# Kernel optimization log

Measured on AMD Instinct MI355X. Metric: run time of the kernel, lower is better.

The kernel has to match this reference:

```python
import jax, jax.numpy as jnp
import numpy as np

N = 65536      # bs * n_graphs * 32 electrodes
E = 1048576    # edges (avg degree 16)
H = 128        # first_hc (out_channels of GatedGraphConv)
IN = 5         # input node features
G = 16         # n_graphs (conv1d in-channels)
ELEC = 32
BS = 128
NC = 3


def setup_inputs() -> dict:
    key = jax.random.key(0)
    ks = jax.random.split(key, 14)
    s = 1.0 / np.sqrt(H)
    x = jax.random.normal(ks[0], (N, IN), dtype=jnp.float32)
    edge_index = jax.random.randint(ks[1], (2, E), 0, N, dtype=jnp.int32)
    edge_attr = jax.random.uniform(ks[2], (E,), dtype=jnp.float32)
    gconv_w = jax.random.normal(ks[3], (2, H, H), dtype=jnp.float32) * s
    gru_w_ih = jax.random.normal(ks[4], (3 * H, H), dtype=jnp.float32) * s
    gru_w_hh = jax.random.normal(ks[5], (3 * H, H), dtype=jnp.float32) * s
    gru_b_ih = jax.random.normal(ks[6], (3 * H,), dtype=jnp.float32) * s
    gru_b_hh = jax.random.normal(ks[7], (3 * H,), dtype=jnp.float32) * s
    conv_w = jax.random.normal(ks[8], (1, G, 3), dtype=jnp.float32) * (1.0 / np.sqrt(G * 3))
    conv_b = jax.random.normal(ks[9], (1,), dtype=jnp.float32) * 0.1
    L = (H - 3) // 2 + 1  # 63
    lin1_w = jax.random.normal(ks[10], (H, ELEC * L), dtype=jnp.float32) * (1.0 / np.sqrt(ELEC * L))
    lin1_b = jnp.zeros((H,), dtype=jnp.float32)
    lin2_w = jax.random.normal(ks[11], (NC, H), dtype=jnp.float32) * s
    lin2_b = jnp.zeros((NC,), dtype=jnp.float32)
    return {"x": x, "edge_index": edge_index, "edge_attr": edge_attr, "bs": BS,
            "gconv_w": gconv_w, "gru_w_ih": gru_w_ih, "gru_w_hh": gru_w_hh,
            "gru_b_ih": gru_b_ih, "gru_b_hh": gru_b_hh,
            "conv_w": conv_w, "conv_b": conv_b,
            "lin1_w": lin1_w, "lin1_b": lin1_b, "lin2_w": lin2_w, "lin2_b": lin2_b}


def _gated_graph_conv(x, edge_index, edge_attr, gconv_w, w_ih, w_hh, b_ih, b_hh):
    n = x.shape[0]
    # pad input features up to H (PyG GatedGraphConv behavior when in < out)
    h = jnp.concatenate([x, jnp.zeros((n, H - x.shape[1]), dtype=x.dtype)], axis=1)
    src, dst = edge_index[0], edge_index[1]
    for i in range(2):  # num_layers = 2
        m = h @ gconv_w[i]                              # [N, H]
        msg = m[src] * edge_attr[:, None]               # gather + edge weight
        agg = jax.ops.segment_sum(msg, dst, num_segments=n)  # scatter-add
        # GRUCell(agg, h)
        gi = agg @ w_ih.T + b_ih
        gh = h @ w_hh.T + b_hh
        i_r, i_z, i_n = jnp.split(gi, 3, axis=1)
        h_r, h_z, h_n = jnp.split(gh, 3, axis=1)
        r = jax.nn.sigmoid(i_r + h_r)
        z = jax.nn.sigmoid(i_z + h_z)
        nn_ = jnp.tanh(i_n + r * h_n)
        h = (1.0 - z) * nn_ + z * h
    return h


def reference(x, edge_index, edge_attr, bs, gconv_w, gru_w_ih, gru_w_hh,
              gru_b_ih, gru_b_hh, conv_w, conv_b, lin1_w, lin1_b, lin2_w, lin2_b):
    h = _gated_graph_conv(x, edge_index, edge_attr, gconv_w,
                          gru_w_ih, gru_w_hh, gru_b_ih, gru_b_hh)
    h = jax.nn.relu(h)  # dropout is identity in eval mode
    g = h.shape[0] // (bs * ELEC)
    # (bs g e) f -> (bs e) g f
    h = h.reshape(bs, g, ELEC, H).transpose(0, 2, 1, 3).reshape(bs * ELEC, g, H)
    h = jax.lax.conv_general_dilated(h, conv_w, window_strides=(2,), padding='VALID',
                                     dimension_numbers=('NCH', 'OIH', 'NCH'))
    h = h + conv_b[None, :, None]
    h = jax.nn.relu(h[:, 0, :])                 # squeeze channel -> [bs*e, L]
    h = h.reshape(bs, -1)                       # (bs e) f -> bs (e f)
    h = jax.nn.relu(h @ lin1_w.T + lin1_b)
    h = h @ lin2_w.T + lin2_b
    return jax.nn.softmax(h, axis=-1)
```

## Files before the change

### kernel.cpp

```cpp
#include <hip/hip_runtime.h>
#include <math.h>

#define NN 65536
#define NE 1048576
#define HH 128
#define ELEC 32
#define BSZ 128
#define NB 512

typedef unsigned short ushort_t;
typedef __bf16 bf16x8 __attribute__((ext_vector_type(8)));
typedef float f32x16 __attribute__((ext_vector_type(16)));

#define MFMA(A, B, C) __builtin_amdgcn_mfma_f32_32x32x16_bf16(A, B, C, 0, 0, 0)

__device__ __forceinline__ float sigm(float x) { return 1.f / (1.f + __expf(-x)); }
__device__ __forceinline__ float tanh_fast(float x) { return 2.f / (1.f + __expf(-2.f * x)) - 1.f; }

__device__ __forceinline__ float bf2f(ushort_t u) {
    union { unsigned int i; float f; } v; v.i = ((unsigned int)u) << 16; return v.f;
}
__device__ __forceinline__ ushort_t f2bf(float f) {
    union { float f; unsigned int i; } v; v.f = f;
    unsigned int r = (v.i + 0x7fffu + ((v.i >> 16) & 1u)) >> 16;
    return (ushort_t)r;
}


__global__ void k_init(const float* __restrict__ x, ushort_t* __restrict__ h) {
    int i = blockIdx.x * 256 + threadIdx.x;
    int n = i >> 7, c = i & 127;
    float v = (c < 5) ? x[n * 5 + c] : 0.f;
    h[(size_t)n * 128 + c] = f2bf(v);
}

__global__ __launch_bounds__(256) void k_bhist(const int* __restrict__ dst,
                                               int* __restrict__ bcnt) {
    __shared__ int hh[NB];
    int t = threadIdx.x;
    hh[t] = 0; hh[t + 256] = 0;
    __syncthreads();
    int e0 = blockIdx.x * 4096;
    #pragma unroll
    for (int i = 0; i < 16; ++i)
        atomicAdd(&hh[dst[e0 + i * 256 + t] >> 7], 1);
    __syncthreads();
    int c0 = hh[t];       if (c0) atomicAdd(&bcnt[t], c0);
    int c1 = hh[t + 256]; if (c1) atomicAdd(&bcnt[t + 256], c1);
}

__global__ void k_bscan(const int* __restrict__ bcnt, int* __restrict__ boffs,
                        int* __restrict__ bcur) {
    __shared__ int s[NB];
    int t = threadIdx.x;
    int v = bcnt[t];
    s[t] = v;
    __syncthreads();
    for (int d = 1; d < NB; d <<= 1) {
        int u = (t >= d) ? s[t - d] : 0;
        __syncthreads();
        s[t] += u;
        __syncthreads();
    }
    int ex = s[t] - v;
    boffs[t] = ex;
    bcur[t] = ex;
    if (t == NB - 1) boffs[NB] = s[t];
}

__global__ __launch_bounds__(256) void k_bpart(const int* __restrict__ src,
        const int* __restrict__ dst, const float* __restrict__ ea,
        int* __restrict__ bcur, uint2* __restrict__ ebkt) {
    __shared__ int lcnt[NB];
    __shared__ int base[NB];
    __shared__ int lcur[NB];
    int t = threadIdx.x;
    lcnt[t] = 0; lcnt[t + 256] = 0;
    lcur[t] = 0; lcur[t + 256] = 0;
    __syncthreads();
    int e0 = blockIdx.x * 4096;
    #pragma unroll
    for (int i = 0; i < 16; ++i)
        atomicAdd(&lcnt[dst[e0 + i * 256 + t] >> 7], 1);
    __syncthreads();
    {
        int c = lcnt[t];
        base[t] = c ? atomicAdd(&bcur[t], c) : 0;
        c = lcnt[t + 256];
        base[t + 256] = c ? atomicAdd(&bcur[t + 256], c) : 0;
    }
    __syncthreads();
    #pragma unroll
    for (int i = 0; i < 16; ++i) {
        int e = e0 + i * 256 + t;
        int d = dst[e];
        int bk = d >> 7;
        int pos = base[bk] + atomicAdd(&lcur[bk], 1);
        uint2 pk;
        pk.x = (unsigned int)src[e] | ((unsigned int)(d & 127) << 16);
        pk.y = __float_as_uint(ea[e]);
        ebkt[pos] = pk;
    }
}

__global__ __launch_bounds__(256) void k_csc(const int* __restrict__ boffs,
        const uint2* __restrict__ ebkt, uint2* __restrict__ epack,
        int* __restrict__ offs) {
    __shared__ int cnt[128];
    __shared__ int s[128];
    __shared__ int base[128];
    int b = blockIdx.x, t = threadIdx.x;
    if (t < 128) cnt[t] = 0;
    __syncthreads();
    int e0 = boffs[b], e1 = boffs[b + 1];
    for (int i = e0 + t; i < e1; i += 256)
        atomicAdd(&cnt[(ebkt[i].x >> 16) & 127], 1);
    __syncthreads();
    if (t < 128) s[t] = cnt[t];
    __syncthreads();
    for (int d = 1; d < 128; d <<= 1) {
        int v = (t < 128 && t >= d) ? s[t - d] : 0;
        __syncthreads();
        if (t < 128) s[t] += v;
        __syncthreads();
    }
    if (t < 128) {
        int bs = e0 + s[t] - cnt[t];
        base[t] = bs;
        offs[b * 128 + t] = bs;
        cnt[t] = 0;
    }
    if (b == 0 && t == 255) offs[NN] = NE;
    __syncthreads();
    for (int i = e0 + t; i < e1; i += 256) {
        uint2 e = ebkt[i];
        int dl = (e.x >> 16) & 127;
        int pos = base[dl] + atomicAdd(&cnt[dl], 1);
        epack[pos] = e;
    }
}

__global__ void k_prep(const float* __restrict__ wih, const float* __restrict__ whh,
                       const float* __restrict__ gw,
                       ushort_t* __restrict__ vp, ushort_t* __restrict__ gp) {
    int b = blockIdx.x, t = threadIdx.x;
    if (b < 512) {
        int i = b * 256 + t;
        int rho = i >> 8, k = i & 255;
        int q = rho >> 7, g = (rho >> 5) & 3, cc = rho & 31;
        int c = q * 32 + cc;
        float v;
        if (g == 0)      v = (k < 128) ? wih[c * 128 + k]          : whh[c * 128 + k - 128];
        else if (g == 1) v = (k < 128) ? wih[(128 + c) * 128 + k]  : whh[(128 + c) * 128 + k - 128];
        else if (g == 2) v = (k < 128) ? wih[(256 + c) * 128 + k]  : 0.f;
        else             v = (k < 128) ? 0.f                       : whh[(256 + c) * 128 + k - 128];
        int ks = k >> 4, lh = (k >> 3) & 1, j = k & 7, lr = cc;
        vp[(size_t)(ks * 16 + q * 4 + g) * 512 + (lh * 32 + lr) * 8 + j] = f2bf(v);
    } else {
        int i = (b - 512) * 256 + t;
        int l = i >> 14, r = i & 16383, c = r >> 7, k = r & 127;
        float v = gw[l * 16384 + k * 128 + c];
        int ct = c >> 5, lr = c & 31;
        int ks = k >> 4, lh = (k >> 3) & 1, j = k & 7;
        gp[(size_t)((l * 8 + ks) * 4 + ct) * 512 + (lh * 32 + lr) * 8 + j] = f2bf(v);
    }
}

__global__ __launch_bounds__(256, 4) void k_mgemm(const ushort_t* __restrict__ gp,
        const ushort_t* __restrict__ h, ushort_t* __restrict__ m) {
    int t = threadIdx.x;
    int lane = t & 63, w = t >> 6;
    int lr = lane & 31, lh = lane >> 5;
    int n0 = blockIdx.x * 128 + w * 32;
    f32x16 acc[4];
    #pragma unroll
    for (int ct = 0; ct < 4; ++ct)
        #pragma unroll
        for (int r = 0; r < 16; ++r) acc[ct][r] = 0.f;
    size_t rowA = (size_t)(n0 + lr) * 128;
    #pragma unroll
    for (int ks = 0; ks < 8; ++ks) {
        int kg = ks * 16 + lh * 8;
        bf16x8 a = *reinterpret_cast<const bf16x8*>(h + rowA + kg);
        #pragma unroll
        for (int ct = 0; ct < 4; ++ct) {
            bf16x8 b = *reinterpret_cast<const bf16x8*>(gp + (size_t)(ks * 4 + ct) * 512 + lane * 8);
            acc[ct] = MFMA(a, b, acc[ct]);
        }
    }
    #pragma unroll
    for (int ct = 0; ct < 4; ++ct)
        #pragma unroll
        for (int r = 0; r < 16; ++r) {
            int row = (r & 3) + 8 * (r >> 2) + 4 * lh;
            m[(size_t)(n0 + row) * 128 + ct * 32 + lr] = f2bf(acc[ct][r]);
        }
}

__global__ __launch_bounds__(256) void k_gather(const ushort_t* __restrict__ m,
        const int* __restrict__ offs, const uint2* __restrict__ epack,
        ushort_t* __restrict__ agg) {
    int n = blockIdx.x * 4 + (threadIdx.x >> 6);
    int lane = threadIdx.x & 63;
    int k0 = offs[n], k1 = offs[n + 1];
    float a0 = 0.f, a1 = 0.f;
    int k = k0;
    if (k < k1 && (k & 1)) {
        uint2 e = epack[k];
        float w = __uint_as_float(e.y);
        ushort2 u = *reinterpret_cast<const ushort2*>(m + (size_t)(e.x & 0xFFFFu) * HH + 2 * lane);
        a0 = fmaf(w, bf2f(u.x), a0);
        a1 = fmaf(w, bf2f(u.y), a1);
        ++k;
    }
    for (; k + 8 <= k1; k += 8) {
        uint4 ea_ = *reinterpret_cast<const uint4*>(epack + k);
        uint4 eb_ = *reinterpret_cast<const uint4*>(epack + k + 2);
        uint4 ec_ = *reinterpret_cast<const uint4*>(epack + k + 4);
        uint4 ed_ = *reinterpret_cast<const uint4*>(epack + k + 6);
        ushort2 u0 = *reinterpret_cast<const ushort2*>(m + (size_t)(ea_.x & 0xFFFFu) * HH + 2 * lane);
        ushort2 u1 = *reinterpret_cast<const ushort2*>(m + (size_t)(ea_.z & 0xFFFFu) * HH + 2 * lane);
        ushort2 u2 = *reinterpret_cast<const ushort2*>(m + (size_t)(eb_.x & 0xFFFFu) * HH + 2 * lane);
        ushort2 u3 = *reinterpret_cast<const ushort2*>(m + (size_t)(eb_.z & 0xFFFFu) * HH + 2 * lane);
        ushort2 u4 = *reinterpret_cast<const ushort2*>(m + (size_t)(ec_.x & 0xFFFFu) * HH + 2 * lane);
        ushort2 u5 = *reinterpret_cast<const ushort2*>(m + (size_t)(ec_.z & 0xFFFFu) * HH + 2 * lane);
        ushort2 u6 = *reinterpret_cast<const ushort2*>(m + (size_t)(ed_.x & 0xFFFFu) * HH + 2 * lane);
        ushort2 u7 = *reinterpret_cast<const ushort2*>(m + (size_t)(ed_.z & 0xFFFFu) * HH + 2 * lane);
        float w0 = __uint_as_float(ea_.y), w1 = __uint_as_float(ea_.w);
        float w2 = __uint_as_float(eb_.y), w3 = __uint_as_float(eb_.w);
        float w4 = __uint_as_float(ec_.y), w5 = __uint_as_float(ec_.w);
        float w6 = __uint_as_float(ed_.y), w7 = __uint_as_float(ed_.w);
        a0 = fmaf(w0, bf2f(u0.x), a0); a1 = fmaf(w0, bf2f(u0.y), a1);
        a0 = fmaf(w1, bf2f(u1.x), a0); a1 = fmaf(w1, bf2f(u1.y), a1);
        a0 = fmaf(w2, bf2f(u2.x), a0); a1 = fmaf(w2, bf2f(u2.y), a1);
        a0 = fmaf(w3, bf2f(u3.x), a0); a1 = fmaf(w3, bf2f(u3.y), a1);
        a0 = fmaf(w4, bf2f(u4.x), a0); a1 = fmaf(w4, bf2f(u4.y), a1);
        a0 = fmaf(w5, bf2f(u5.x), a0); a1 = fmaf(w5, bf2f(u5.y), a1);
        a0 = fmaf(w6, bf2f(u6.x), a0); a1 = fmaf(w6, bf2f(u6.y), a1);
        a0 = fmaf(w7, bf2f(u7.x), a0); a1 = fmaf(w7, bf2f(u7.y), a1);
    }
    for (; k + 2 <= k1; k += 2) {
        uint4 e01 = *reinterpret_cast<const uint4*>(epack + k);
        ushort2 u0 = *reinterpret_cast<const ushort2*>(m + (size_t)(e01.x & 0xFFFFu) * HH + 2 * lane);
        ushort2 u1 = *reinterpret_cast<const ushort2*>(m + (size_t)(e01.z & 0xFFFFu) * HH + 2 * lane);
        float w0 = __uint_as_float(e01.y), w1 = __uint_as_float(e01.w);
        a0 = fmaf(w0, bf2f(u0.x), a0); a1 = fmaf(w0, bf2f(u0.y), a1);
        a0 = fmaf(w1, bf2f(u1.x), a0); a1 = fmaf(w1, bf2f(u1.y), a1);
    }
    if (k < k1) {
        uint2 e = epack[k];
        float w = __uint_as_float(e.y);
        ushort2 u = *reinterpret_cast<const ushort2*>(m + (size_t)(e.x & 0xFFFFu) * HH + 2 * lane);
        a0 = fmaf(w, bf2f(u.x), a0);
        a1 = fmaf(w, bf2f(u.y), a1);
    }
    ushort2 o; o.x = f2bf(a0); o.y = f2bf(a1);
    *reinterpret_cast<ushort2*>(agg + (size_t)n * 128 + 2 * lane) = o;
}

__global__ __launch_bounds__(512, 4) void k_gru(const ushort_t* __restrict__ vp,
        const ushort_t* __restrict__ agg, ushort_t* __restrict__ h,
        const float* __restrict__ bih, const float* __restrict__ bhh) {
    int t = threadIdx.x;
    int lane = t & 63, w = t >> 6;
    int q = w >> 1, s = w & 1;
    int lr = lane & 31, lh = lane >> 5;
    int n0 = blockIdx.x * 64 + s * 32;
    f32x16 acc[4];
    #pragma unroll
    for (int g = 0; g < 4; ++g)
        #pragma unroll
        for (int r = 0; r < 16; ++r) acc[g][r] = 0.f;

    size_t rowA = (size_t)(n0 + lr) * 128;
    #pragma unroll
    for (int ks = 0; ks < 16; ++ks) {
        bf16x8 a;
        if (ks < 8) a = *reinterpret_cast<const bf16x8*>(agg + rowA + ks * 16 + lh * 8);
        else        a = *reinterpret_cast<const bf16x8*>(h + rowA + (ks - 8) * 16 + lh * 8);
        #pragma unroll
        for (int g = 0; g < 4; ++g) {
            bf16x8 b = *reinterpret_cast<const bf16x8*>(vp + (size_t)(ks * 16 + q * 4 + g) * 512 + lane * 8);
            acc[g] = MFMA(a, b, acc[g]);
        }
    }

    __syncthreads();

    int c = q * 32 + lr;
    float brz = bih[c] + bhh[c];
    float bzz = bih[128 + c] + bhh[128 + c];
    float bin = bih[256 + c];
    float bhn = bhh[256 + c];
    #pragma unroll
    for (int r = 0; r < 16; ++r) {
        int node = n0 + (r & 3) + 8 * (r >> 2) + 4 * lh;
        float rg = sigm(acc[0][r] + brz);
        float zg = sigm(acc[1][r] + bzz);
        float nn = tanh_fast(acc[2][r] + bin + rg * (acc[3][r] + bhn));
        size_t idx = (size_t)node * 128 + c;
        float hold = bf2f(h[idx]);
        float hnew = (1.f - zg) * nn + zg * hold;
        h[idx] = f2bf(hnew);
    }
}

__global__ __launch_bounds__(64) void k_conv(const ushort_t* __restrict__ h,
        const float* __restrict__ cw, const float* __restrict__ cb,
        float* __restrict__ co) {
    __shared__ float tile[16 * 128];
    __shared__ float w[48];
    int be = blockIdx.x;
    int b = be >> 5, e = be & 31;
    int t = threadIdx.x;
    if (t < 48) w[t] = cw[t];
    #pragma unroll
    for (int i = 0; i < 8; ++i) {
        int f = t + i * 64;
        int g = f >> 5, c4 = f & 31;
        size_t idx = (size_t)(b * 512 + g * 32 + e) * 128 + c4 * 4;
        ushort4 vh4 = *reinterpret_cast<const ushort4*>(h + idx);
        float* dst = tile + g * 128 + c4 * 4;
        dst[0] = fmaxf(bf2f(vh4.x), 0.f);
        dst[1] = fmaxf(bf2f(vh4.y), 0.f);
        dst[2] = fmaxf(bf2f(vh4.z), 0.f);
        dst[3] = fmaxf(bf2f(vh4.w), 0.f);
    }
    __syncthreads();
    if (t < 63) {
        float s = cb[0];
        #pragma unroll
        for (int g = 0; g < 16; ++g) {
            const float* p = tile + g * 128 + 2 * t;
            s = fmaf(p[0], w[g * 3 + 0], s);
            s = fmaf(p[1], w[g * 3 + 1], s);
            s = fmaf(p[2], w[g * 3 + 2], s);
        }
        co[b * 2016 + e * 63 + t] = fmaxf(s, 0.f);
    }
}

__global__ __launch_bounds__(128) void k_lin1(const float* __restrict__ co,
        const float* __restrict__ w, const float* __restrict__ bias,
        float* __restrict__ fc1) {
    __shared__ float v[2016];
    int b = blockIdx.x, t = threadIdx.x;
    for (int i = t; i < 2016; i += 128) v[i] = co[b * 2016 + i];
    __syncthreads();
    float s = bias[t];
    const float* wr = w + t * 2016;
    for (int k = 0; k < 2016; k += 4) {
        float4 wv = *reinterpret_cast<const float4*>(wr + k);
        s = fmaf(wv.x, v[k + 0], s);
        s = fmaf(wv.y, v[k + 1], s);
        s = fmaf(wv.z, v[k + 2], s);
        s = fmaf(wv.w, v[k + 3], s);
    }
    fc1[b * 128 + t] = fmaxf(s, 0.f);
}

__global__ __launch_bounds__(128) void k_lin2(const float* __restrict__ fc1,
        const float* __restrict__ w, const float* __restrict__ bias,
        float* __restrict__ out) {
    int b = threadIdx.x;
    float s0 = bias[0], s1 = bias[1], s2 = bias[2];
    const float* v = fc1 + b * 128;
    for (int k = 0; k < 128; ++k) {
        float x = v[k];
        s0 = fmaf(x, w[k], s0);
        s1 = fmaf(x, w[128 + k], s1);
        s2 = fmaf(x, w[256 + k], s2);
    }
    float mx = fmaxf(s0, fmaxf(s1, s2));
    float e0 = __expf(s0 - mx), e1 = __expf(s1 - mx), e2 = __expf(s2 - mx);
    float inv = 1.f / (e0 + e1 + e2);
    out[b * 3 + 0] = e0 * inv;
    out[b * 3 + 1] = e1 * inv;
    out[b * 3 + 2] = e2 * inv;
}

extern "C" void kernel_launch(void* const* d_in, const int* in_sizes, int n_in,
                              void* d_out, int out_size, void* d_ws, size_t ws_size,
                              hipStream_t stream) {
    const float* x   = (const float*)d_in[0];
    const int*   ei  = (const int*)d_in[1];
    const float* ea  = (const float*)d_in[2];
    const float* gw  = (const float*)d_in[4];
    const float* wih = (const float*)d_in[5];
    const float* whh = (const float*)d_in[6];
    const float* bih = (const float*)d_in[7];
    const float* bhh = (const float*)d_in[8];
    const float* cw  = (const float*)d_in[9];
    const float* cb  = (const float*)d_in[10];
    const float* l1w = (const float*)d_in[11];
    const float* l1b = (const float*)d_in[12];
    const float* l2w = (const float*)d_in[13];
    const float* l2b = (const float*)d_in[14];
    float* out = (float*)d_out;

    char* p = (char*)d_ws;
    ushort_t* h   = (ushort_t*)p; p += (size_t)NN * 128 * 2;
    ushort_t* agg = (ushort_t*)p; p += (size_t)NN * 128 * 2;
    ushort_t* vp  = (ushort_t*)p; p += 512 * 256 * 2;
    ushort_t* gp  = (ushort_t*)p; p += 2 * 128 * 128 * 2;
    ushort_t* m   = (ushort_t*)p; p += (size_t)NN * HH * 2;
    uint2* ebkt   = (uint2*)p;   p += (size_t)NE * 8;
    uint2* epack  = (uint2*)p;   p += (size_t)NE * 8;
    float* co  = (float*)p; p += (size_t)BSZ * 2016 * 4;
    float* fc1 = (float*)p; p += (size_t)BSZ * HH * 4;
    int* bcnt  = (int*)p; p += NB * 4;
    int* boffs = (int*)p; p += (NB + 1) * 4;
    int* bcur  = (int*)p; p += NB * 4;
    int* offs  = (int*)p; p += (size_t)(NN + 1) * 4;

    const int* src = ei;
    const int* dst = ei + NE;

    k_prep<<<640, 256, 0, stream>>>(wih, whh, gw, vp, gp);
    hipMemsetAsync(bcnt, 0, NB * 4, stream);
    k_bhist<<<256, 256, 0, stream>>>(dst, bcnt);
    k_bscan<<<1, 512, 0, stream>>>(bcnt, boffs, bcur);
    k_bpart<<<256, 256, 0, stream>>>(src, dst, ea, bcur, ebkt);
    k_csc<<<NB, 256, 0, stream>>>(boffs, ebkt, epack, offs);
    k_init<<<(NN * 128) / 256, 256, 0, stream>>>(x, h);

    for (int layer = 0; layer < 2; ++layer) {
        k_mgemm<<<NN / 128, 256, 0, stream>>>(gp + (size_t)layer * 16384, h, m);
        k_gather<<<NN / 4, 256, 0, stream>>>(m, offs, epack, agg);
        k_gru<<<NN / 64, 512, 0, stream>>>(vp, agg, h, bih, bhh);
    }

    k_conv<<<BSZ * ELEC, 64, 0, stream>>>(h, cw, cb, co);
    k_lin1<<<BSZ, 128, 0, stream>>>(co, l1w, l1b, fc1);
    k_lin2<<<1, 128, 0, stream>>>(fc1, l2w, l2b, out);
}
```

Baseline: 377.8 us.

## Split lin1 across K with transposed weights and atomics; raise GRU occupancy bound

lin1 previously ran on only 128 blocks, each thread streaming a 2016-long weight row with strided per-thread access. The weight is now transposed once in the prep kernel so reads are coalesced across output channels. The K dimension is split into 8 chunks, giving 1024 blocks whose partial sums are combined with atomicAdd into a zeroed fc1. Bias and ReLU move into lin2. Separately, the GRU kernel's launch bounds ask for 8 blocks per SM instead of 4, which may force register spills. The transpose adds about 1 MB of extra traffic, and float atomics make the sum order nondeterministic.

```diff
diff --git a/kernel.cpp b/kernel.cpp
--- a/kernel.cpp
+++ b/kernel.cpp
@@ -141,8 +141,9 @@
 }
 
 __global__ void k_prep(const float* __restrict__ wih, const float* __restrict__ whh,
-                       const float* __restrict__ gw,
-                       ushort_t* __restrict__ vp, ushort_t* __restrict__ gp) {
+                       const float* __restrict__ gw, const float* __restrict__ l1w,
+                       ushort_t* __restrict__ vp, ushort_t* __restrict__ gp,
+                       float* __restrict__ wt) {
     int b = blockIdx.x, t = threadIdx.x;
     if (b < 512) {
         int i = b * 256 + t;
@@ -156,13 +157,17 @@
         else             v = (k < 128) ? 0.f                       : whh[(256 + c) * 128 + k - 128];
         int ks = k >> 4, lh = (k >> 3) & 1, j = k & 7, lr = cc;
         vp[(size_t)(ks * 16 + q * 4 + g) * 512 + (lh * 32 + lr) * 8 + j] = f2bf(v);
-    } else {
+    } else if (b < 640) {
         int i = (b - 512) * 256 + t;
         int l = i >> 14, r = i & 16383, c = r >> 7, k = r & 127;
         float v = gw[l * 16384 + k * 128 + c];
         int ct = c >> 5, lr = c & 31;
         int ks = k >> 4, lh = (k >> 3) & 1, j = k & 7;
         gp[(size_t)((l * 8 + ks) * 4 + ct) * 512 + (lh * 32 + lr) * 8 + j] = f2bf(v);
+    } else {
+        int i = (b - 640) * 256 + t;
+        int k = i >> 7, c = i & 127;
+        wt[i] = l1w[c * 2016 + k];
     }
 }
 
@@ -258,7 +263,7 @@
     *reinterpret_cast<ushort2*>(agg + (size_t)n * 128 + 2 * lane) = o;
 }
 
-__global__ __launch_bounds__(512, 4) void k_gru(const ushort_t* __restrict__ vp,
+__global__ __launch_bounds__(512, 8) void k_gru(const ushort_t* __restrict__ vp,
         const ushort_t* __restrict__ agg, ushort_t* __restrict__ h,
         const float* __restrict__ bih, const float* __restrict__ bhh) {
     int t = threadIdx.x;
@@ -341,32 +346,27 @@
 }
 
 __global__ __launch_bounds__(128) void k_lin1(const float* __restrict__ co,
-        const float* __restrict__ w, const float* __restrict__ bias,
-        float* __restrict__ fc1) {
-    __shared__ float v[2016];
-    int b = blockIdx.x, t = threadIdx.x;
-    for (int i = t; i < 2016; i += 128) v[i] = co[b * 2016 + i];
-    __syncthreads();
-    float s = bias[t];
-    const float* wr = w + t * 2016;
-    for (int k = 0; k < 2016; k += 4) {
-        float4 wv = *reinterpret_cast<const float4*>(wr + k);
-        s = fmaf(wv.x, v[k + 0], s);
-        s = fmaf(wv.y, v[k + 1], s);
-        s = fmaf(wv.z, v[k + 2], s);
-        s = fmaf(wv.w, v[k + 3], s);
-    }
-    fc1[b * 128 + t] = fmaxf(s, 0.f);
+        const float* __restrict__ wt, float* __restrict__ fc1) {
+    int b = blockIdx.x >> 3;
+    int ks = blockIdx.x & 7;
+    int c = threadIdx.x;
+    const float* cb_ = co + b * 2016 + ks * 252;
+    const float* wb = wt + (ks * 252) * 128 + c;
+    float s = 0.f;
+    #pragma unroll 4
+    for (int k = 0; k < 252; ++k)
+        s = fmaf(wb[k * 128], cb_[k], s);
+    atomicAdd(&fc1[b * 128 + c], s);
 }
 
 __global__ __launch_bounds__(128) void k_lin2(const float* __restrict__ fc1,
-        const float* __restrict__ w, const float* __restrict__ bias,
-        float* __restrict__ out) {
+        const float* __restrict__ l1b, const float* __restrict__ w,
+        const float* __restrict__ bias, float* __restrict__ out) {
     int b = threadIdx.x;
     float s0 = bias[0], s1 = bias[1], s2 = bias[2];
     const float* v = fc1 + b * 128;
     for (int k = 0; k < 128; ++k) {
-        float x = v[k];
+        float x = fmaxf(v[k] + l1b[k], 0.f);
         s0 = fmaf(x, w[k], s0);
         s1 = fmaf(x, w[128 + k], s1);
         s2 = fmaf(x, w[256 + k], s2);
@@ -406,6 +406,7 @@
     ushort_t* m   = (ushort_t*)p; p += (size_t)NN * HH * 2;
     uint2* ebkt   = (uint2*)p;   p += (size_t)NE * 8;
     uint2* epack  = (uint2*)p;   p += (size_t)NE * 8;
+    float* wt  = (float*)p; p += 2016 * 128 * 4;
     float* co  = (float*)p; p += (size_t)BSZ * 2016 * 4;
     float* fc1 = (float*)p; p += (size_t)BSZ * HH * 4;
     int* bcnt  = (int*)p; p += NB * 4;
@@ -416,8 +417,9 @@
     const int* src = ei;
     const int* dst = ei + NE;
 
-    k_prep<<<640, 256, 0, stream>>>(wih, whh, gw, vp, gp);
+    k_prep<<<1648, 256, 0, stream>>>(wih, whh, gw, l1w, vp, gp, wt);
     hipMemsetAsync(bcnt, 0, NB * 4, stream);
+    hipMemsetAsync(fc1, 0, (size_t)BSZ * HH * 4, stream);
     k_bhist<<<256, 256, 0, stream>>>(dst, bcnt);
     k_bscan<<<1, 512, 0, stream>>>(bcnt, boffs, bcur);
     k_bpart<<<256, 256, 0, stream>>>(src, dst, ea, bcur, ebkt);
@@ -431,6 +433,6 @@
     }
 
     k_conv<<<BSZ * ELEC, 64, 0, stream>>>(h, cw, cb, co);
-    k_lin1<<<BSZ, 128, 0, stream>>>(co, l1w, l1b, fc1);
-    k_lin2<<<1, 128, 0, stream>>>(fc1, l2w, l2b, out);
-}
+    k_lin1<<<BSZ * 8, 128, 0, stream>>>(co, wt, fc1);
+    k_lin2<<<1, 128, 0, stream>>>(fc1, l1b, l2w, l2b, out);
+}
```

After: 986.2 us. +161.0%, slower.
